# Performance work log

Measured on AMD Instinct MI355X. Metric: run time of the kernel, lower is better.

## Reference

```python
import jax, jax.numpy as jnp
import numpy as np

B, N, IN_F, OUT_F, H = 4, 1024, 256, 256, 8
HID = OUT_F // H  # 32
ALPHA = 0.2  # leaky relu negative slope


def setup_inputs() -> dict:
    key = jax.random.key(0)
    k1, k2, k3, k4 = jax.random.split(key, 4)
    h = jax.random.normal(k1, (B, N, IN_F), dtype=jnp.float32)
    # linear: in_features -> n_heads*n_hidden, no bias (stored as [in, out])
    W = jax.random.normal(k2, (IN_F, H * HID), dtype=jnp.float32) / np.sqrt(IN_F)
    # attn: Linear(2*n_hidden, 1, bias=False), shared across heads
    attn_w = jax.random.normal(k3, (2 * HID,), dtype=jnp.float32) / np.sqrt(2 * HID)
    # random dense adjacency (p=0.5) plus self loops, broadcast over heads
    u = jax.random.uniform(k4, (B, N, N, 1), dtype=jnp.float32)
    adj_mat = jnp.maximum((u < 0.5).astype(jnp.float32), jnp.eye(N, dtype=jnp.float32)[None, :, :, None])
    return {"h": h, "adj_mat": adj_mat, "W": W, "attn_w": attn_w}


def reference(h, adj_mat, W, attn_w):
    # g: [b, n, h, d]
    g = (h @ W).reshape(B, N, H, HID)
    # attn(concat(g_i, g_j)) decomposes: e[b,i,j,h] = <attn_w[:HID], g_i> + <attn_w[HID:], g_j>
    # (exactly the math of the repeat/repeat_interleave/cat + 1-wide linear, without the N^2 concat)
    e_i = jnp.einsum('bnhd,d->bnh', g, attn_w[:HID])   # g_repeat_interleave part (index i)
    e_j = jnp.einsum('bnhd,d->bnh', g, attn_w[HID:])   # g_repeat part (index j)
    e = e_i[:, :, None, :] + e_j[:, None, :, :]        # [b, i, j, h]
    e = jnp.where(e >= 0, e, ALPHA * e)                # LeakyReLU(alpha)
    e = jnp.where(adj_mat == 0, -jnp.inf, e)           # masked_fill
    a = jax.nn.softmax(e, axis=1)                      # faithful: original uses Softmax(dim=1)
    # dropout p acts as identity in eval mode / p=0
    out = jnp.einsum('bijh,bjhd->bihd', a, g)          # [b, i, h, d]
    return out.reshape(B, N, H * HID)                  # is_concat=True
```

## Files before the change

### kernel.cpp

```cpp
#include <hip/hip_runtime.h>
#include <math.h>

#define BB 4
#define NN 1024
#define HH 8
#define NROW (BB*NN)

typedef short s8v __attribute__((ext_vector_type(8)));
typedef float f4v __attribute__((ext_vector_type(4)));

__device__ __forceinline__ short bf16rne(float f) {
    unsigned u = __float_as_uint(f);
    u += 0x7FFF + ((u >> 16) & 1u);
    return (short)(u >> 16);
}
__device__ __forceinline__ unsigned pk2(float a, float b) {
    return ((unsigned)(unsigned short)bf16rne(a)) |
           (((unsigned)(unsigned short)bf16rne(b)) << 16);
}

__global__ __launch_bounds__(256) void k_gemm_ei(const float* __restrict__ hm,
                                                 const float* __restrict__ W,
                                                 const float* __restrict__ aw,
                                                 short* __restrict__ Gt,
                                                 float* __restrict__ EFi,
                                                 float* __restrict__ EFjt) {
    __shared__ __align__(16) float hs[8][256];
    __shared__ float aws[64];
    const int row0 = blockIdx.x * 8;
    const int t = threadIdx.x;
    if (t < 64) aws[t] = aw[t];
    const float4* h4 = (const float4*)(hm + row0 * 256);
    float4* hs4 = (float4*)&hs[0][0];
    hs4[t] = h4[t];
    hs4[t + 256] = h4[t + 256];
    __syncthreads();

    float acc[8];
#pragma unroll
    for (int r = 0; r < 8; ++r) acc[r] = 0.f;
    for (int k4 = 0; k4 < 64; ++k4) {
        const float w0 = W[(4 * k4 + 0) * 256 + t];
        const float w1 = W[(4 * k4 + 1) * 256 + t];
        const float w2 = W[(4 * k4 + 2) * 256 + t];
        const float w3 = W[(4 * k4 + 3) * 256 + t];
#pragma unroll
        for (int r = 0; r < 8; ++r) {
            const float4 hv = *(const float4*)&hs[r][4 * k4];
            acc[r] = fmaf(hv.x, w0, acc[r]);
            acc[r] = fmaf(hv.y, w1, acc[r]);
            acc[r] = fmaf(hv.z, w2, acc[r]);
            acc[r] = fmaf(hv.w, w3, acc[r]);
        }
    }
    const int d = t & 31, hh = t >> 5;
    const int b = row0 >> 10;

    {
        const int n0 = row0 & (NN - 1);
        short* dst = Gt + ((size_t)((b * 8 + hh) * 32 + (n0 >> 5))) * 1024 +
                     d * 32 + (n0 & 31);
        uint4 w;
        w.x = pk2(acc[0], acc[1]);
        w.y = pk2(acc[2], acc[3]);
        w.z = pk2(acc[4], acc[5]);
        w.w = pk2(acc[6], acc[7]);
        *(uint4*)dst = w;
    }

#pragma unroll
    for (int r = 0; r < 8; ++r) {
        float vi = acc[r] * aws[d];
        float vj = acc[r] * aws[32 + d];
#pragma unroll
        for (int mm = 1; mm < 32; mm <<= 1) {
            vi += __shfl_xor(vi, mm);
            vj += __shfl_xor(vj, mm);
        }
        if (d == 0) {
            const int row = row0 + r;
            const int n = row & (NN - 1);
            *(float2*)&EFi[(size_t)row * 16 + hh * 2] =
                make_float2(__expf(vi), __expf(0.2f * vi));
            EFjt[((size_t)(b * 8 + hh) * 2 + 0) * NN + n] = __expf(vj);
            EFjt[((size_t)(b * 8 + hh) * 2 + 1) * NN + n] = __expf(0.2f * vj);
        }
    }
}

__global__ __launch_bounds__(256) void k_s(const float* __restrict__ adj,
                                           const float* __restrict__ EFi,
                                           const float* __restrict__ EFjt,
                                           float* __restrict__ ps) {
    __shared__ __align__(16) float eis[128 * 16];
    __shared__ float sp[4][8][64];
    const int bx = blockIdx.x;
    const int b = bx >> 7, jc = (bx >> 3) & 15, ic = bx & 7;
    const int j0 = jc * 64, i0 = ic * 128;
    const int t = threadIdx.x;

    const float4* src4 = (const float4*)(EFi + (size_t)(b * NN + i0) * 16);
    ((float4*)eis)[t] = src4[t];
    ((float4*)eis)[t + 256] = src4[t + 256];

    const int ii = t >> 6, jj = t & 63;
    const float* ejb = EFjt + (size_t)b * 16 * NN + j0 + jj;
    const float ejE0 = ejb[0 * NN],  ejF0 = ejb[1 * NN];
    const float ejE1 = ejb[2 * NN],  ejF1 = ejb[3 * NN];
    const float ejE2 = ejb[4 * NN],  ejF2 = ejb[5 * NN];
    const float ejE3 = ejb[6 * NN],  ejF3 = ejb[7 * NN];
    const float ejE4 = ejb[8 * NN],  ejF4 = ejb[9 * NN];
    const float ejE5 = ejb[10 * NN], ejF5 = ejb[11 * NN];
    const float ejE6 = ejb[12 * NN], ejF6 = ejb[13 * NN];
    const float ejE7 = ejb[14 * NN], ejF7 = ejb[15 * NN];
    __syncthreads();

    float s0 = 0.f, s1 = 0.f, s2 = 0.f, s3 = 0.f;
    float s4 = 0.f, s5 = 0.f, s6 = 0.f, s7 = 0.f;
    const float* adjp = adj + (size_t)b * NN * NN + j0 + jj;
    for (int i = ii; i < 128; i += 4) {
        const float a = adjp[(size_t)(i0 + i) * NN];
        const float4 x0 = *(const float4*)&eis[i * 16];
        const float4 x1 = *(const float4*)&eis[i * 16 + 4];
        const float4 x2 = *(const float4*)&eis[i * 16 + 8];
        const float4 x3 = *(const float4*)&eis[i * 16 + 12];
        s0 = fmaf(a, fmaxf(x0.x * ejE0, x0.y * ejF0), s0);
        s1 = fmaf(a, fmaxf(x0.z * ejE1, x0.w * ejF1), s1);
        s2 = fmaf(a, fmaxf(x1.x * ejE2, x1.y * ejF2), s2);
        s3 = fmaf(a, fmaxf(x1.z * ejE3, x1.w * ejF3), s3);
        s4 = fmaf(a, fmaxf(x2.x * ejE4, x2.y * ejF4), s4);
        s5 = fmaf(a, fmaxf(x2.z * ejE5, x2.w * ejF5), s5);
        s6 = fmaf(a, fmaxf(x3.x * ejE6, x3.y * ejF6), s6);
        s7 = fmaf(a, fmaxf(x3.z * ejE7, x3.w * ejF7), s7);
    }
    sp[ii][0][jj] = s0; sp[ii][1][jj] = s1; sp[ii][2][jj] = s2; sp[ii][3][jj] = s3;
    sp[ii][4][jj] = s4; sp[ii][5][jj] = s5; sp[ii][6][jj] = s6; sp[ii][7][jj] = s7;
    __syncthreads();
#pragma unroll
    for (int k = 0; k < 2; ++k) {
        const int idx = t * 2 + k;
        const int jjo = idx >> 3, hq = idx & 7;
        const float sv =
            sp[0][hq][jjo] + sp[1][hq][jjo] + sp[2][hq][jjo] + sp[3][hq][jjo];
        ps[((size_t)(ic * 4 + b) * 8 + hq) * 1024 + j0 + jjo] = sv;
    }
}

__global__ __launch_bounds__(256) void k_nrm(const float* __restrict__ ps,
                                             const float* __restrict__ EFjt,
                                             float* __restrict__ EFjtn) {
    const int t = blockIdx.x * 256 + threadIdx.x;
    const f4v* p4 = (const f4v*)ps;
    const f4v d = p4[t]            + p4[t + 1 * 8192] + p4[t + 2 * 8192] +
                  p4[t + 3 * 8192] + p4[t + 4 * 8192] + p4[t + 5 * 8192] +
                  p4[t + 6 * 8192] + p4[t + 7 * 8192];
    const int bh = t >> 8, j4 = t & 255;
    const f4v* e4 = (const f4v*)EFjt;
    f4v* o4 = (f4v*)EFjtn;
    f4v E = e4[(size_t)(bh * 2 + 0) * 256 + j4];
    f4v F = e4[(size_t)(bh * 2 + 1) * 256 + j4];
    E[0] /= d[0]; E[1] /= d[1]; E[2] /= d[2]; E[3] /= d[3];
    F[0] /= d[0]; F[1] /= d[1]; F[2] /= d[2]; F[3] /= d[3];
    o4[(size_t)(bh * 2 + 0) * 256 + j4] = E;
    o4[(size_t)(bh * 2 + 1) * 256 + j4] = F;
}

__global__ __launch_bounds__(256) void k_out_mfma(const float* __restrict__ adj,
                                                  const short* __restrict__ Gt,
                                                  const float* __restrict__ EFi,
                                                  const float* __restrict__ EFjtn,
                                                  float* __restrict__ out) {
    __shared__ short gts[4][4][32][40];
    __shared__ float ejt[4][2][128];
    const int bx = blockIdx.x;
    const int hs = bx >> 8, b = (bx >> 6) & 3, i0 = (bx & 63) * 16;
    const int t = threadIdx.x;
    const int wave = t >> 6, lane = t & 63;
    const int m = lane & 15, q = lane >> 4;
    const int h = hs * 4 + wave;

    const float2 eif = *(const float2*)&EFi[(size_t)(b * NN + i0 + m) * 16 + h * 2];
    const float EiV = eif.x, FiV = eif.y;
    f4v acc0 = {0.f, 0.f, 0.f, 0.f}, acc1 = {0.f, 0.f, 0.f, 0.f};

    const float* adjrow = adj + (size_t)b * NN * NN + (size_t)(i0 + m) * NN;
    const float4* gtg4 = (const float4*)Gt;
    const float4* ejt4 = (const float4*)(EFjtn + (size_t)b * 8 * 2 * NN);

    for (int s = 0; s < 8; ++s) {
        float4 g0, g1, g2, g3, g4, g5, g6, g7;
#define LG(k)                                                                     \
        {                                                                         \
            const int u = t + 256 * (k);                                          \
            g##k = gtg4[(size_t)(b * 8 + hs * 4 + (u >> 9)) * 4096 + s * 512 +    \
                        (u & 511)];                                               \
        }
        LG(0) LG(1) LG(2) LG(3) LG(4) LG(5) LG(6) LG(7)
#undef LG
        f4v a0, a1, a2, a3, a4, a5, a6, a7;
#define LA(k2, lt, half)                                                          \
        a##k2 = *(const f4v*)&adjrow[s * 128 + (lt) * 32 + q * 8 + (half) * 4];
        LA(0, 0, 0) LA(1, 0, 1) LA(2, 1, 0) LA(3, 1, 1)
        LA(4, 2, 0) LA(5, 2, 1) LA(6, 3, 0) LA(7, 3, 1)
#undef LA
        const float4 ev =
            ejt4[(size_t)((hs * 4 + (t >> 6)) * 2 + ((t >> 5) & 1)) * 256 +
                 s * 32 + (t & 31)];
        __syncthreads();
#define SG(k)                                                                     \
        {                                                                         \
            const int u = t + 256 * (k);                                          \
            char* dstp = (char*)gts + (u >> 9) * 10240 + ((u >> 7) & 3) * 2560 +  \
                         ((u >> 2) & 31) * 80 + (u & 3) * 16;                     \
            *(float4*)dstp = g##k;                                                \
        }
        SG(0) SG(1) SG(2) SG(3) SG(4) SG(5) SG(6) SG(7)
#undef SG
        *(float4*)&ejt[t >> 6][(t >> 5) & 1][(t & 31) * 4] = ev;
        __syncthreads();

#define LT(lt, aA, aB)                                                            \
        {                                                                         \
            const f4v ejA = *(const f4v*)&ejt[wave][0][(lt) * 32 + q * 8];        \
            const f4v ejB = *(const f4v*)&ejt[wave][0][(lt) * 32 + q * 8 + 4];    \
            const f4v fjA = *(const f4v*)&ejt[wave][1][(lt) * 32 + q * 8];        \
            const f4v fjB = *(const f4v*)&ejt[wave][1][(lt) * 32 + q * 8 + 4];    \
            const float p0 = aA[0] * fmaxf(EiV * ejA[0], FiV * fjA[0]);           \
            const float p1 = aA[1] * fmaxf(EiV * ejA[1], FiV * fjA[1]);           \
            const float p2 = aA[2] * fmaxf(EiV * ejA[2], FiV * fjA[2]);           \
            const float p3 = aA[3] * fmaxf(EiV * ejA[3], FiV * fjA[3]);           \
            const float p4 = aB[0] * fmaxf(EiV * ejB[0], FiV * fjB[0]);           \
            const float p5 = aB[1] * fmaxf(EiV * ejB[1], FiV * fjB[1]);           \
            const float p6 = aB[2] * fmaxf(EiV * ejB[2], FiV * fjB[2]);           \
            const float p7 = aB[3] * fmaxf(EiV * ejB[3], FiV * fjB[3]);           \
            unsigned w0, w1, w2, w3;                                              \
            asm("v_cvt_pk_bf16_f32 %0, %1, %2" : "=v"(w0) : "v"(p0), "v"(p1));    \
            asm("v_cvt_pk_bf16_f32 %0, %1, %2" : "=v"(w1) : "v"(p2), "v"(p3));    \
            asm("v_cvt_pk_bf16_f32 %0, %1, %2" : "=v"(w2) : "v"(p4), "v"(p5));    \
            asm("v_cvt_pk_bf16_f32 %0, %1, %2" : "=v"(w3) : "v"(p6), "v"(p7));    \
            union { unsigned u[4]; s8v v; } Au;                                   \
            Au.u[0] = w0; Au.u[1] = w1; Au.u[2] = w2; Au.u[3] = w3;               \
            const s8v A = Au.v;                                                   \
            const s8v B0 = *(const s8v*)&gts[wave][lt][m][q * 8];                 \
            const s8v B1 = *(const s8v*)&gts[wave][lt][m + 16][q * 8];            \
            acc0 = __builtin_amdgcn_mfma_f32_16x16x32_bf16(A, B0, acc0, 0, 0, 0); \
            acc1 = __builtin_amdgcn_mfma_f32_16x16x32_bf16(A, B1, acc1, 0, 0, 0); \
        }
        LT(0, a0, a1) LT(1, a2, a3) LT(2, a4, a5) LT(3, a6, a7)
#undef LT
    }

    float* op = out + (size_t)(b * NN + i0) * 256;
#pragma unroll
    for (int r = 0; r < 4; ++r) {
        const int row = q * 4 + r;
        op[(size_t)row * 256 + h * 32 + m] = acc0[r];
        op[(size_t)row * 256 + h * 32 + 16 + m] = acc1[r];
    }
}

extern "C" void kernel_launch(void* const* d_in, const int* in_sizes, int n_in,
                              void* d_out, int out_size, void* d_ws, size_t ws_size,
                              hipStream_t stream) {
    const float* h      = (const float*)d_in[0];
    const float* adj    = (const float*)d_in[1];
    const float* W      = (const float*)d_in[2];
    const float* attn_w = (const float*)d_in[3];
    float* out = (float*)d_out;

    float* ws = (float*)d_ws;
    short* Gt    = (short*)ws;
    float* EFi   = ws + 1048576;
    float* EFjt  = EFi + NROW * 16;
    float* ps    = EFjt + NROW * 16;
    float* EFjtn = ps + 8 * NROW * 8;

    k_gemm_ei<<<NROW / 8, 256, 0, stream>>>(h, W, attn_w, Gt, EFi, EFjt);
    k_s<<<512, 256, 0, stream>>>(adj, EFi, EFjt, ps);
    k_nrm<<<32, 256, 0, stream>>>(ps, EFjt, EFjtn);
    k_out_mfma<<<512, 256, 0, stream>>>(adj, Gt, EFi, EFjtn, out);
}
```

Baseline: 123.6 us.

## Split output kernel into one-wave blocks per head reading B operands directly

Rewrites the aggregation MFMA kernel so each 64-thread block handles a single head and 16 rows. It reads the Gt tiles and the normalized e_j/f_j vectors straight from global memory instead of staging them through shared memory with two barriers per step. The block count grows fourfold, and bf16 packing moves from the inline asm cvt instruction to a software round-to-nearest routine. In exchange, each adjacency row is now read by eight blocks instead of two, which adds more L2/HBM traffic on the dominant adj reads.

Result: slower. 132.1 us (+6.9%).

```diff
diff --git a/kernel.cpp b/kernel.cpp
--- a/kernel.cpp
+++ b/kernel.cpp
@@ -165,89 +165,52 @@
     o4[(size_t)(bh * 2 + 1) * 256 + j4] = F;
 }
 
-__global__ __launch_bounds__(256) void k_out_mfma(const float* __restrict__ adj,
-                                                  const short* __restrict__ Gt,
-                                                  const float* __restrict__ EFi,
-                                                  const float* __restrict__ EFjtn,
-                                                  float* __restrict__ out) {
-    __shared__ short gts[4][4][32][40];
-    __shared__ float ejt[4][2][128];
+__global__ __launch_bounds__(64) void k_out_mfma(const float* __restrict__ adj,
+                                                 const short* __restrict__ Gt,
+                                                 const float* __restrict__ EFi,
+                                                 const float* __restrict__ EFjtn,
+                                                 float* __restrict__ out) {
     const int bx = blockIdx.x;
-    const int hs = bx >> 8, b = (bx >> 6) & 3, i0 = (bx & 63) * 16;
-    const int t = threadIdx.x;
-    const int wave = t >> 6, lane = t & 63;
+    const int h = bx >> 8, b = (bx >> 6) & 3, i0 = (bx & 63) * 16;
+    const int lane = threadIdx.x;
     const int m = lane & 15, q = lane >> 4;
-    const int h = hs * 4 + wave;
+    const int bh = b * 8 + h;
 
     const float2 eif = *(const float2*)&EFi[(size_t)(b * NN + i0 + m) * 16 + h * 2];
     const float EiV = eif.x, FiV = eif.y;
     f4v acc0 = {0.f, 0.f, 0.f, 0.f}, acc1 = {0.f, 0.f, 0.f, 0.f};
 
     const float* adjrow = adj + (size_t)b * NN * NN + (size_t)(i0 + m) * NN;
-    const float4* gtg4 = (const float4*)Gt;
-    const float4* ejt4 = (const float4*)(EFjtn + (size_t)b * 8 * 2 * NN);
-
-    for (int s = 0; s < 8; ++s) {
-        float4 g0, g1, g2, g3, g4, g5, g6, g7;
-#define LG(k)                                                                     \
-        {                                                                         \
-            const int u = t + 256 * (k);                                          \
-            g##k = gtg4[(size_t)(b * 8 + hs * 4 + (u >> 9)) * 4096 + s * 512 +    \
-                        (u & 511)];                                               \
-        }
-        LG(0) LG(1) LG(2) LG(3) LG(4) LG(5) LG(6) LG(7)
-#undef LG
-        f4v a0, a1, a2, a3, a4, a5, a6, a7;
-#define LA(k2, lt, half)                                                          \
-        a##k2 = *(const f4v*)&adjrow[s * 128 + (lt) * 32 + q * 8 + (half) * 4];
-        LA(0, 0, 0) LA(1, 0, 1) LA(2, 1, 0) LA(3, 1, 1)
-        LA(4, 2, 0) LA(5, 2, 1) LA(6, 3, 0) LA(7, 3, 1)
-#undef LA
-        const float4 ev =
-            ejt4[(size_t)((hs * 4 + (t >> 6)) * 2 + ((t >> 5) & 1)) * 256 +
-                 s * 32 + (t & 31)];
-        __syncthreads();
-#define SG(k)                                                                     \
-        {                                                                         \
-            const int u = t + 256 * (k);                                          \
-            char* dstp = (char*)gts + (u >> 9) * 10240 + ((u >> 7) & 3) * 2560 +  \
-                         ((u >> 2) & 31) * 80 + (u & 3) * 16;                     \
-            *(float4*)dstp = g##k;                                                \
-        }
-        SG(0) SG(1) SG(2) SG(3) SG(4) SG(5) SG(6) SG(7)
-#undef SG
-        *(float4*)&ejt[t >> 6][(t >> 5) & 1][(t & 31) * 4] = ev;
-        __syncthreads();
-
-#define LT(lt, aA, aB)                                                            \
-        {                                                                         \
-            const f4v ejA = *(const f4v*)&ejt[wave][0][(lt) * 32 + q * 8];        \
-            const f4v ejB = *(const f4v*)&ejt[wave][0][(lt) * 32 + q * 8 + 4];    \
-            const f4v fjA = *(const f4v*)&ejt[wave][1][(lt) * 32 + q * 8];        \
-            const f4v fjB = *(const f4v*)&ejt[wave][1][(lt) * 32 + q * 8 + 4];    \
-            const float p0 = aA[0] * fmaxf(EiV * ejA[0], FiV * fjA[0]);           \
-            const float p1 = aA[1] * fmaxf(EiV * ejA[1], FiV * fjA[1]);           \
-            const float p2 = aA[2] * fmaxf(EiV * ejA[2], FiV * fjA[2]);           \
-            const float p3 = aA[3] * fmaxf(EiV * ejA[3], FiV * fjA[3]);           \
-            const float p4 = aB[0] * fmaxf(EiV * ejB[0], FiV * fjB[0]);           \
-            const float p5 = aB[1] * fmaxf(EiV * ejB[1], FiV * fjB[1]);           \
-            const float p6 = aB[2] * fmaxf(EiV * ejB[2], FiV * fjB[2]);           \
-            const float p7 = aB[3] * fmaxf(EiV * ejB[3], FiV * fjB[3]);           \
-            unsigned w0, w1, w2, w3;                                              \
-            asm("v_cvt_pk_bf16_f32 %0, %1, %2" : "=v"(w0) : "v"(p0), "v"(p1));    \
-            asm("v_cvt_pk_bf16_f32 %0, %1, %2" : "=v"(w1) : "v"(p2), "v"(p3));    \
-            asm("v_cvt_pk_bf16_f32 %0, %1, %2" : "=v"(w2) : "v"(p4), "v"(p5));    \
-            asm("v_cvt_pk_bf16_f32 %0, %1, %2" : "=v"(w3) : "v"(p6), "v"(p7));    \
-            union { unsigned u[4]; s8v v; } Au;                                   \
-            Au.u[0] = w0; Au.u[1] = w1; Au.u[2] = w2; Au.u[3] = w3;               \
-            const s8v A = Au.v;                                                   \
-            const s8v B0 = *(const s8v*)&gts[wave][lt][m][q * 8];                 \
-            const s8v B1 = *(const s8v*)&gts[wave][lt][m + 16][q * 8];            \
-            acc0 = __builtin_amdgcn_mfma_f32_16x16x32_bf16(A, B0, acc0, 0, 0, 0); \
-            acc1 = __builtin_amdgcn_mfma_f32_16x16x32_bf16(A, B1, acc1, 0, 0, 0); \
-        }
-        LT(0, a0, a1) LT(1, a2, a3) LT(2, a4, a5) LT(3, a6, a7)
-#undef LT
+    const float* ejrow  = EFjtn + ((size_t)bh * 2 + 0) * NN;
+    const float* fjrow  = EFjtn + ((size_t)bh * 2 + 1) * NN;
+    const short* gtb    = Gt + (size_t)bh * 32768;
+
+    for (int jt = 0; jt < 32; ++jt) {
+        const int jb = jt * 32 + q * 8;
+        const f4v aA  = *(const f4v*)&adjrow[jb];
+        const f4v aB  = *(const f4v*)&adjrow[jb + 4];
+        const f4v ejA = *(const f4v*)&ejrow[jb];
+        const f4v ejB = *(const f4v*)&ejrow[jb + 4];
+        const f4v fjA = *(const f4v*)&fjrow[jb];
+        const f4v fjB = *(const f4v*)&fjrow[jb + 4];
+        const s8v B0 = *(const s8v*)&gtb[(jt * 32 + m) * 32 + q * 8];
+        const s8v B1 = *(const s8v*)&gtb[(jt * 32 + m + 16) * 32 + q * 8];
+
+        const float p0 = aA[0] * fmaxf(EiV * ejA[0], FiV * fjA[0]);
+        const float p1 = aA[1] * fmaxf(EiV * ejA[1], FiV * fjA[1]);
+        const float p2 = aA[2] * fmaxf(EiV * ejA[2], FiV * fjA[2]);
+        const float p3 = aA[3] * fmaxf(EiV * ejA[3], FiV * fjA[3]);
+        const float p4 = aB[0] * fmaxf(EiV * ejB[0], FiV * fjB[0]);
+        const float p5 = aB[1] * fmaxf(EiV * ejB[1], FiV * fjB[1]);
+        const float p6 = aB[2] * fmaxf(EiV * ejB[2], FiV * fjB[2]);
+        const float p7 = aB[3] * fmaxf(EiV * ejB[3], FiV * fjB[3]);
+        union { unsigned u[4]; s8v v; } Au;
+        Au.u[0] = pk2(p0, p1);
+        Au.u[1] = pk2(p2, p3);
+        Au.u[2] = pk2(p4, p5);
+        Au.u[3] = pk2(p6, p7);
+        acc0 = __builtin_amdgcn_mfma_f32_16x16x32_bf16(Au.v, B0, acc0, 0, 0, 0);
+        acc1 = __builtin_amdgcn_mfma_f32_16x16x32_bf16(Au.v, B1, acc1, 0, 0, 0);
     }
 
     float* op = out + (size_t)(b * NN + i0) * 256;
@@ -278,5 +241,5 @@
     k_gemm_ei<<<NROW / 8, 256, 0, stream>>>(h, W, attn_w, Gt, EFi, EFjt);
     k_s<<<512, 256, 0, stream>>>(adj, EFi, EFjt, ps);
     k_nrm<<<32, 256, 0, stream>>>(ps, EFjt, EFjtn);
-    k_out_mfma<<<512, 256, 0, stream>>>(adj, Gt, EFi, EFjtn, out);
-}
+    k_out_mfma<<<2048, 64, 0, stream>>>(adj, Gt, EFi, EFjtn, out);
+}
```
